# Kernel tuning notes

Measured on AMD Instinct MI355X. Metric: run time of the kernel, lower is better.

## Reference

```python
import jax, jax.numpy as jnp
import numpy as np

B, T, C, H = 2, 2048, 2048, 16
HD = C // H  # 128 head dim
ROPE_BASE = 10000.0


def setup_inputs() -> dict:
    key = jax.random.key(0)
    k0, k1, k2 = jax.random.split(key, 3)
    x = jax.random.normal(k0, (B, T, C), dtype=jnp.float32)
    W_attn = jax.random.normal(k1, (C, 3 * C), dtype=jnp.float32) * 0.02
    b_attn = jnp.zeros((3 * C,), dtype=jnp.float32)
    W_proj = jax.random.normal(k2, (C, C), dtype=jnp.float32) * 0.02
    b_proj = jnp.zeros((C,), dtype=jnp.float32)
    # freqs_cis = exp(i * t * theta_j), represented as (cos, sin), shape [T, HD//2]
    inv_freq = 1.0 / (ROPE_BASE ** (jnp.arange(0, HD, 2, dtype=jnp.float32) / HD))
    freqs = jnp.outer(jnp.arange(T, dtype=jnp.float32), inv_freq)
    return {"x": x, "W_attn": W_attn, "b_attn": b_attn, "W_proj": W_proj,
            "b_proj": b_proj, "cos": jnp.cos(freqs), "sin": jnp.sin(freqs)}


def _apply_rope(v, cos, sin):
    # v: [B, T, H, HD]; pairs (v[..., 2i], v[..., 2i+1]) rotated by angle freqs[t, i]
    vr = v.reshape(v.shape[:-1] + (-1, 2))
    x0, x1 = vr[..., 0], vr[..., 1]
    c = cos[None, :, None, :]  # [1, T, 1, HD//2]
    s = sin[None, :, None, :]
    o0 = x0 * c - x1 * s
    o1 = x0 * s + x1 * c
    return jnp.stack([o0, o1], axis=-1).reshape(v.shape)


def reference(x, W_attn, b_attn, W_proj, b_proj, cos, sin):
    Bv, Tv, Cv = x.shape
    qkv = x @ W_attn + b_attn                      # [B, T, 3C]
    q, k, v = jnp.split(qkv, 3, axis=-1)
    q = q.reshape(Bv, Tv, H, HD)
    k = k.reshape(Bv, Tv, H, HD)
    v = v.reshape(Bv, Tv, H, HD)
    q = _apply_rope(q, cos, sin)
    k = _apply_rope(k, cos, sin)
    scale = 1.0 / jnp.sqrt(jnp.float32(HD))
    att = jnp.einsum('bqhd,bkhd->bhqk', q, k) * scale
    causal = jnp.tril(jnp.ones((Tv, Tv), dtype=bool))
    att = jnp.where(causal[None, None], att, jnp.finfo(att.dtype).min)
    att = jax.nn.softmax(att, axis=-1)
    y = jnp.einsum('bhqk,bkhd->bqhd', att, v).reshape(Bv, Tv, Cv)
    return y @ W_proj + b_proj
```

## Files before the change

kernel.cpp:

```cpp
#include <hip/hip_runtime.h>

typedef unsigned short u16;
typedef __attribute__((ext_vector_type(8))) short short8;
typedef __attribute__((ext_vector_type(4))) float f32x4;

#define TSEQ 2048
#define NHEAD 16
#define HDIM 128

__device__ __forceinline__ u16 f2bf(float x) {
    unsigned u = __float_as_uint(x);
    return (u16)((u + 0x7fffu + ((u >> 16) & 1u)) >> 16);
}
__device__ __forceinline__ float b2f(u16 h) {
    return __uint_as_float(((unsigned)h) << 16);
}
__device__ __forceinline__ void async16(const void* g, void* l) {
    __builtin_amdgcn_global_load_lds((__attribute__((address_space(1))) void*)(void*)g,
                                     (__attribute__((address_space(3))) void*)l, 16, 0, 0);
}
__device__ __forceinline__ f32x4 zero4() {
    f32x4 z = {0.f, 0.f, 0.f, 0.f};
    return z;
}

template <int CTRL>
__device__ __forceinline__ float dppf(float x) {
    return __int_as_float(__builtin_amdgcn_mov_dpp(__float_as_int(x), CTRL, 0xf, 0xf, true));
}
__device__ __forceinline__ float dpp_max16(float x) {
    x = fmaxf(x, dppf<0xB1>(x));
    x = fmaxf(x, dppf<0x4E>(x));
    x = fmaxf(x, dppf<0x141>(x));
    x = fmaxf(x, dppf<0x140>(x));
    return x;
}
__device__ __forceinline__ float dpp_sum16(float x) {
    x += dppf<0xB1>(x);
    x += dppf<0x4E>(x);
    x += dppf<0x141>(x);
    x += dppf<0x140>(x);
    return x;
}

__global__ void cast_bf16(const float4* __restrict__ in, ushort4* __restrict__ out, int n4) {
    int i = blockIdx.x * 256 + threadIdx.x;
    if (i < n4) {
        float4 v = in[i];
        ushort4 o;
        o.x = f2bf(v.x); o.y = f2bf(v.y); o.z = f2bf(v.z); o.w = f2bf(v.w);
        out[i] = o;
    }
}

__global__ void transpose_cast(const float* __restrict__ in, u16* __restrict__ out, int K, int N) {
    __shared__ float tile[64][65];
    int n0 = blockIdx.x * 64, k0 = blockIdx.y * 64;
    int tx = threadIdx.x & 63, ty = threadIdx.x >> 6;
#pragma unroll
    for (int i = 0; i < 16; i++) {
        int r = ty + i * 4;
        tile[r][tx] = in[(size_t)(k0 + r) * N + n0 + tx];
    }
    __syncthreads();
#pragma unroll
    for (int i = 0; i < 16; i++) {
        int r = ty + i * 4;
        out[(size_t)(n0 + r) * K + k0 + tx] = f2bf(tile[tx][r]);
    }
}

template <int MODE>
__global__ __launch_bounds__(256) void gemm_bt(
    const u16* __restrict__ A, const u16* __restrict__ Bt, const float* __restrict__ bias,
    float* __restrict__ outf, u16* __restrict__ qb, u16* __restrict__ kb, u16* __restrict__ vb,
    int M, int N, int K) {
    __shared__ u16 As[128 * 32];
    __shared__ u16 Bs[128 * 32];
    const int tid = threadIdx.x;
    const int wave = tid >> 6, lane = tid & 63;
    const int low = lane & 15, quad = lane >> 4;
    const int m0 = blockIdx.y * 128, n0 = blockIdx.x * 128;
    const int wm = (wave >> 1) * 64, wn = (wave & 1) * 64;
    const int ldr = lane >> 2;
    const int ldc = (lane & 3) * 8;

    f32x4 acc[4][4];
#pragma unroll
    for (int i = 0; i < 4; i++)
#pragma unroll
        for (int j = 0; j < 4; j++) acc[i][j] = zero4();

    for (int k0 = 0; k0 < K; k0 += 32) {
#pragma unroll
        for (int c = 0; c < 2; ++c) {
            const int chunk = wave * 2 + c;
            const int row = chunk * 16 + ldr;
            async16(A + (size_t)(m0 + row) * K + k0 + ldc, As + chunk * 512);
            async16(Bt + (size_t)(n0 + row) * K + k0 + ldc, Bs + chunk * 512);
        }
        __syncthreads();
        short8 af[4], bfv[4];
#pragma unroll
        for (int i = 0; i < 4; i++) af[i] = *(const short8*)(As + (wm + i * 16 + low) * 32 + quad * 8);
#pragma unroll
        for (int j = 0; j < 4; j++) bfv[j] = *(const short8*)(Bs + (wn + j * 16 + low) * 32 + quad * 8);
#pragma unroll
        for (int i = 0; i < 4; i++)
#pragma unroll
            for (int j = 0; j < 4; j++)
                acc[i][j] = __builtin_amdgcn_mfma_f32_16x16x32_bf16(af[i], bfv[j], acc[i][j], 0, 0, 0);
        __syncthreads();
    }

#pragma unroll
    for (int j = 0; j < 4; j++) {
        const int ng = n0 + wn + j * 16 + low;
        const float bv = bias[ng];
#pragma unroll
        for (int i = 0; i < 4; i++) {
            const int rbase = m0 + wm + i * 16 + quad * 4;
#pragma unroll
            for (int r = 0; r < 4; r++) {
                float v = acc[i][j][r] + bv;
                int rowg = rbase + r;
                if (MODE == 1) {
                    outf[(size_t)rowg * N + ng] = v;
                } else {
                    int which = ng >> 11;
                    int hd = ng & 2047;
                    int bq = rowg >> 11, t = rowg & 2047;
                    u16* dst = (which == 0) ? qb : (which == 1) ? kb : vb;
                    dst[(((size_t)(bq * NHEAD + (hd >> 7))) * TSEQ + t) * HDIM + (hd & 127)] = f2bf(v);
                }
            }
        }
    }
}

__global__ void rope_inplace(u16* __restrict__ qb, u16* __restrict__ kb,
                             const float* __restrict__ cosp, const float* __restrict__ sinp) {
    int idx = blockIdx.x * 256 + threadIdx.x;
    int i = idx & 63;
    int bt = idx >> 6;
    int t = bt & (TSEQ - 1);
    size_t o = (size_t)bt * HDIM + 2 * i;
    float c = cosp[t * 64 + i], s = sinp[t * 64 + i];
    float q0 = b2f(qb[o]), q1 = b2f(qb[o + 1]);
    qb[o] = f2bf(q0 * c - q1 * s);
    qb[o + 1] = f2bf(q0 * s + q1 * c);
    float k0 = b2f(kb[o]), k1 = b2f(kb[o + 1]);
    kb[o] = f2bf(k0 * c - k1 * s);
    kb[o + 1] = f2bf(k0 * s + k1 * c);
}

__global__ void vtrans(const u16* __restrict__ vtmp, u16* __restrict__ vT) {
    __shared__ u16 tile[64][66];
    int bid = blockIdx.x;
    int tt = bid & 31;
    int dt = (bid >> 5) & 1;
    int bh = bid >> 6;
    int t0 = tt * 64, d0 = dt * 64;
    int tx = threadIdx.x & 63, ty = threadIdx.x >> 6;
    size_t ibase = ((size_t)bh * TSEQ + t0) * HDIM + d0;
#pragma unroll
    for (int i = 0; i < 16; i++) {
        int r = ty + i * 4;
        tile[r][tx] = vtmp[ibase + (size_t)r * HDIM + tx];
    }
    __syncthreads();
    size_t obase = ((size_t)bh * HDIM + d0) * TSEQ + t0;
#pragma unroll
    for (int i = 0; i < 16; i++) {
        int r = ty + i * 4;
        vT[obase + (size_t)r * TSEQ + tx] = tile[tx][r];
    }
}

__global__ __launch_bounds__(256) void flash_attn(const u16* __restrict__ qb, const u16* __restrict__ kb,
                                                  const u16* __restrict__ vT, u16* __restrict__ y) {
    __shared__ u16 Ks[64 * 128];
    __shared__ u16 Vs[128 * 64];
    __shared__ u16 Ps[4][16 * 72];
    const int tid = threadIdx.x;
    const int wave = tid >> 6, lane = tid & 63;
    const int low = lane & 15, quad = lane >> 4;
    const int bh = blockIdx.x;
    const int qt = 31 - blockIdx.y;
    const int q0 = qt * 64 + wave * 16;
    const float scale2 = 0.08838834764831845f * 1.44269504088896f;

    const u16* Qp = qb + ((size_t)bh * TSEQ + q0) * HDIM;
    short8 qf[4];
#pragma unroll
    for (int c = 0; c < 4; c++) qf[c] = *(const short8*)(Qp + (size_t)low * HDIM + c * 32 + quad * 8);

    f32x4 o[8];
#pragma unroll
    for (int d = 0; d < 8; d++) o[d] = zero4();
    float m_i[4], l_i[4];
#pragma unroll
    for (int r = 0; r < 4; r++) { m_i[r] = -1e30f; l_i[r] = 0.f; }

    const u16* Kb = kb + (size_t)bh * TSEQ * HDIM;
    const u16* Vb = vT + (size_t)bh * HDIM * TSEQ;
    u16* Pw = &Ps[wave][0];
    const int ntiles = qt + 1;

    const int krow = tid >> 4, kchunk = tid & 15;
    const int vrow = tid >> 3, vchunk = tid & 7;

    for (int kt = 0; kt < ntiles; ++kt) {
        const int kv0 = kt * 64;
#pragma unroll
        for (int j = 0; j < 4; j++) {
            const int row = j * 16 + krow;
            const int gc = kchunk ^ (row & 7);
            async16(Kb + (size_t)(kv0 + row) * HDIM + gc * 8, Ks + row * 128 + kchunk * 8);
        }
#pragma unroll
        for (int j = 0; j < 4; j++) {
            const int d = j * 32 + vrow;
            const int gc = vchunk ^ (d & 7);
            async16(Vb + (size_t)d * TSEQ + kv0 + gc * 8, Vs + d * 64 + vchunk * 8);
        }
        __syncthreads();

        f32x4 s[4];
#pragma unroll
        for (int h = 0; h < 4; h++) s[h] = zero4();
#pragma unroll
        for (int h = 0; h < 4; h++) {
            const int row = h * 16 + low;
#pragma unroll
            for (int c = 0; c < 4; c++) {
                const int cc = c * 4 + quad;
                short8 kf = *(const short8*)(Ks + row * 128 + (cc ^ (row & 7)) * 8);
                s[h] = __builtin_amdgcn_mfma_f32_16x16x32_bf16(qf[c], kf, s[h], 0, 0, 0);
            }
        }

        float alpha[4];
#pragma unroll
        for (int r = 0; r < 4; r++) {
            const int qg = q0 + quad * 4 + r;
            float sv[4];
#pragma unroll
            for (int h = 0; h < 4; h++)
                sv[h] = (kv0 + h * 16 + low <= qg) ? s[h][r] * scale2 : -1e30f;
            float mx = fmaxf(fmaxf(sv[0], sv[1]), fmaxf(sv[2], sv[3]));
            mx = dpp_max16(mx);
            float mnew = fmaxf(m_i[r], mx);
            alpha[r] = exp2f(m_i[r] - mnew);
            m_i[r] = mnew;
            float p0 = exp2f(sv[0] - mnew);
            float p1 = exp2f(sv[1] - mnew);
            float p2 = exp2f(sv[2] - mnew);
            float p3 = exp2f(sv[3] - mnew);
            float rs = (p0 + p1) + (p2 + p3);
            rs = dpp_sum16(rs);
            l_i[r] = l_i[r] * alpha[r] + rs;
            const int prow = (quad * 4 + r) * 72;
            Pw[prow + low] = f2bf(p0);
            Pw[prow + 16 + low] = f2bf(p1);
            Pw[prow + 32 + low] = f2bf(p2);
            Pw[prow + 48 + low] = f2bf(p3);
        }
        __threadfence_block();

#pragma unroll
        for (int d = 0; d < 8; ++d)
#pragma unroll
            for (int r = 0; r < 4; r++) o[d][r] *= alpha[r];

#pragma unroll
        for (int kc = 0; kc < 2; kc++) {
            short8 pf = *(const short8*)(Pw + low * 72 + kc * 32 + quad * 8);
#pragma unroll
            for (int dd = 0; dd < 8; ++dd) {
                const int vr = dd * 16 + low;
                const int cc = kc * 4 + quad;
                short8 vf = *(const short8*)(Vs + vr * 64 + (cc ^ (vr & 7)) * 8);
                o[dd] = __builtin_amdgcn_mfma_f32_16x16x32_bf16(pf, vf, o[dd], 0, 0, 0);
            }
        }
        __syncthreads();
    }

    const int b = bh >> 4, h = bh & 15;
#pragma unroll
    for (int r = 0; r < 4; r++) {
        float inv = 1.0f / l_i[r];
        size_t row = (size_t)(b * TSEQ + q0 + quad * 4 + r);
        u16* yp = y + row * 2048 + h * HDIM;
#pragma unroll
        for (int d = 0; d < 8; ++d) yp[d * 16 + low] = f2bf(o[d][r] * inv);
    }
}

extern "C" void kernel_launch(void* const* d_in, const int* in_sizes, int n_in,
                              void* d_out, int out_size, void* d_ws, size_t ws_size,
                              hipStream_t stream) {
    const float* x = (const float*)d_in[0];
    const float* Wa = (const float*)d_in[1];
    const float* ba = (const float*)d_in[2];
    const float* Wp = (const float*)d_in[3];
    const float* bp = (const float*)d_in[4];
    const float* cs = (const float*)d_in[5];
    const float* sn = (const float*)d_in[6];
    float* out = (float*)d_out;

    u16* xb = (u16*)d_ws;
    u16* Wab = xb + 8388608;
    u16* Wpb = Wab + 12582912;
    u16* qb = Wpb + 4194304;
    u16* kb = qb + 8388608;
    u16* vtmp = kb + 8388608;
    u16* vT = vtmp + 8388608;
    u16* y = xb;

    cast_bf16<<<8192, 256, 0, stream>>>((const float4*)x, (ushort4*)xb, 2097152);
    transpose_cast<<<dim3(96, 32), 256, 0, stream>>>(Wa, Wab, 2048, 6144);
    transpose_cast<<<dim3(32, 32), 256, 0, stream>>>(Wp, Wpb, 2048, 2048);
    gemm_bt<0><<<dim3(48, 32), 256, 0, stream>>>(xb, Wab, ba, nullptr, qb, kb, vtmp, 4096, 6144, 2048);
    rope_inplace<<<16384, 256, 0, stream>>>(qb, kb, cs, sn);
    vtrans<<<2048, 256, 0, stream>>>(vtmp, vT);
    flash_attn<<<dim3(32, 32), 256, 0, stream>>>(qb, kb, vT, y);
    gemm_bt<1><<<dim3(16, 32), 256, 0, stream>>>(y, Wpb, bp, out, nullptr, nullptr, nullptr, 4096, 2048, 2048);
}
```

Baseline: 463.7 us.

## Fuse RoPE and V transpose into QKV GEMM epilogue via LDS staging

The QKV GEMM epilogue now stages each 128x128 output tile through shared memory. For Q and K tiles it applies RoPE and writes vectorized 16-byte rows. For V tiles it writes the transposed layout directly. This removes the separate rope_inplace and vtrans kernels, their global round trips, and the vtmp buffer. In exchange the epilogue gains extra barriers, a larger shared-memory footprint, and cos/sin loads inside the GEMM.

```diff
diff --git a/kernel.cpp b/kernel.cpp
--- a/kernel.cpp
+++ b/kernel.cpp
@@ -73,10 +73,12 @@
 template <int MODE>
 __global__ __launch_bounds__(256) void gemm_bt(
     const u16* __restrict__ A, const u16* __restrict__ Bt, const float* __restrict__ bias,
-    float* __restrict__ outf, u16* __restrict__ qb, u16* __restrict__ kb, u16* __restrict__ vb,
+    float* __restrict__ outf, u16* __restrict__ qb, u16* __restrict__ kb, u16* __restrict__ vT,
+    const float* __restrict__ cosp, const float* __restrict__ sinp,
     int M, int N, int K) {
-    __shared__ u16 As[128 * 32];
-    __shared__ u16 Bs[128 * 32];
+    __shared__ __align__(16) u16 smem[8704];
+    u16* As = smem;
+    u16* Bs = smem + 4096;
     const int tid = threadIdx.x;
     const int wave = tid >> 6, lane = tid & 63;
     const int low = lane & 15, quad = lane >> 4;
@@ -113,67 +115,92 @@
         __syncthreads();
     }
 
-#pragma unroll
-    for (int j = 0; j < 4; j++) {
-        const int ng = n0 + wn + j * 16 + low;
-        const float bv = bias[ng];
-#pragma unroll
-        for (int i = 0; i < 4; i++) {
-            const int rbase = m0 + wm + i * 16 + quad * 4;
-#pragma unroll
-            for (int r = 0; r < 4; r++) {
-                float v = acc[i][j][r] + bv;
-                int rowg = rbase + r;
-                if (MODE == 1) {
-                    outf[(size_t)rowg * N + ng] = v;
-                } else {
-                    int which = ng >> 11;
-                    int hd = ng & 2047;
-                    int bq = rowg >> 11, t = rowg & 2047;
-                    u16* dst = (which == 0) ? qb : (which == 1) ? kb : vb;
-                    dst[(((size_t)(bq * NHEAD + (hd >> 7))) * TSEQ + t) * HDIM + (hd & 127)] = f2bf(v);
-                }
-            }
-        }
-    }
-}
-
-__global__ void rope_inplace(u16* __restrict__ qb, u16* __restrict__ kb,
-                             const float* __restrict__ cosp, const float* __restrict__ sinp) {
-    int idx = blockIdx.x * 256 + threadIdx.x;
-    int i = idx & 63;
-    int bt = idx >> 6;
-    int t = bt & (TSEQ - 1);
-    size_t o = (size_t)bt * HDIM + 2 * i;
-    float c = cosp[t * 64 + i], s = sinp[t * 64 + i];
-    float q0 = b2f(qb[o]), q1 = b2f(qb[o + 1]);
-    qb[o] = f2bf(q0 * c - q1 * s);
-    qb[o + 1] = f2bf(q0 * s + q1 * c);
-    float k0 = b2f(kb[o]), k1 = b2f(kb[o + 1]);
-    kb[o] = f2bf(k0 * c - k1 * s);
-    kb[o + 1] = f2bf(k0 * s + k1 * c);
-}
-
-__global__ void vtrans(const u16* __restrict__ vtmp, u16* __restrict__ vT) {
-    __shared__ u16 tile[64][66];
-    int bid = blockIdx.x;
-    int tt = bid & 31;
-    int dt = (bid >> 5) & 1;
-    int bh = bid >> 6;
-    int t0 = tt * 64, d0 = dt * 64;
-    int tx = threadIdx.x & 63, ty = threadIdx.x >> 6;
-    size_t ibase = ((size_t)bh * TSEQ + t0) * HDIM + d0;
-#pragma unroll
-    for (int i = 0; i < 16; i++) {
-        int r = ty + i * 4;
-        tile[r][tx] = vtmp[ibase + (size_t)r * HDIM + tx];
-    }
-    __syncthreads();
-    size_t obase = ((size_t)bh * HDIM + d0) * TSEQ + t0;
-#pragma unroll
-    for (int i = 0; i < 16; i++) {
-        int r = ty + i * 4;
-        vT[obase + (size_t)r * TSEQ + tx] = tile[tx][r];
+    if (MODE == 1) {
+#pragma unroll
+        for (int j = 0; j < 4; j++) {
+            const int ng = n0 + wn + j * 16 + low;
+            const float bv = bias[ng];
+#pragma unroll
+            for (int i = 0; i < 4; i++) {
+                const int rbase = m0 + wm + i * 16 + quad * 4;
+#pragma unroll
+                for (int r = 0; r < 4; r++)
+                    outf[(size_t)(rbase + r) * N + ng] = acc[i][j][r] + bv;
+            }
+        }
+        return;
+    }
+
+    const int which = n0 >> 11;
+    const int h = (n0 & 2047) >> 7;
+    const int b = m0 >> 11, t0 = m0 & 2047;
+    float bv[4];
+#pragma unroll
+    for (int j = 0; j < 4; j++) bv[j] = bias[n0 + wn + j * 16 + low];
+    u16* epi = smem;
+
+    if (which < 2) {
+        u16* dst = (which == 0 ? qb : kb) + (((size_t)(b * NHEAD + h)) * TSEQ + t0) * HDIM;
+#pragma unroll
+        for (int pass = 0; pass < 2; pass++) {
+            if ((wave >> 1) == pass) {
+#pragma unroll
+                for (int i = 0; i < 4; i++)
+#pragma unroll
+                    for (int j = 0; j < 4; j++)
+#pragma unroll
+                        for (int r = 0; r < 4; r++)
+                            epi[(i * 16 + quad * 4 + r) * 136 + wn + j * 16 + low] =
+                                f2bf(acc[i][j][r] + bv[j]);
+            }
+            __syncthreads();
+            const int row = tid >> 2, dp = (tid & 3) * 32;
+            const int t = t0 + pass * 64 + row;
+            u16 vals[32];
+#pragma unroll
+            for (int q = 0; q < 4; q++)
+                *(short8*)(vals + q * 8) = *(const short8*)(epi + row * 136 + dp + q * 8);
+            float cs4[16], sn4[16];
+#pragma unroll
+            for (int q = 0; q < 4; q++) {
+                *(float4*)(cs4 + q * 4) = *(const float4*)(cosp + (size_t)t * 64 + (dp >> 1) + q * 4);
+                *(float4*)(sn4 + q * 4) = *(const float4*)(sinp + (size_t)t * 64 + (dp >> 1) + q * 4);
+            }
+            u16 outv[32];
+#pragma unroll
+            for (int p = 0; p < 16; p++) {
+                float x0 = b2f(vals[2 * p]), x1 = b2f(vals[2 * p + 1]);
+                outv[2 * p] = f2bf(x0 * cs4[p] - x1 * sn4[p]);
+                outv[2 * p + 1] = f2bf(x0 * sn4[p] + x1 * cs4[p]);
+            }
+            u16* dr = dst + (size_t)(pass * 64 + row) * HDIM + dp;
+#pragma unroll
+            for (int q = 0; q < 4; q++)
+                *(short8*)(dr + q * 8) = *(const short8*)(outv + q * 8);
+            __syncthreads();
+        }
+    } else {
+        u16* dst = vT + ((size_t)(b * NHEAD + h)) * HDIM * TSEQ + t0;
+#pragma unroll
+        for (int pass = 0; pass < 2; pass++) {
+            if ((wave & 1) == pass) {
+#pragma unroll
+                for (int i = 0; i < 4; i++)
+#pragma unroll
+                    for (int j = 0; j < 4; j++)
+#pragma unroll
+                        for (int r = 0; r < 4; r++)
+                            epi[(j * 16 + low) * 136 + wm + i * 16 + quad * 4 + r] =
+                                f2bf(acc[i][j][r] + bv[j]);
+            }
+            __syncthreads();
+            const int drow = tid >> 2, tc = (tid & 3) * 32;
+            u16* dr = dst + (size_t)(pass * 64 + drow) * TSEQ + tc;
+#pragma unroll
+            for (int q = 0; q < 4; q++)
+                *(short8*)(dr + q * 8) = *(const short8*)(epi + drow * 136 + tc + q * 8);
+            __syncthreads();
+        }
     }
 }
 
@@ -315,16 +342,13 @@
     u16* Wpb = Wab + 12582912;
     u16* qb = Wpb + 4194304;
     u16* kb = qb + 8388608;
-    u16* vtmp = kb + 8388608;
-    u16* vT = vtmp + 8388608;
+    u16* vT = kb + 8388608;
     u16* y = xb;
 
     cast_bf16<<<8192, 256, 0, stream>>>((const float4*)x, (ushort4*)xb, 2097152);
     transpose_cast<<<dim3(96, 32), 256, 0, stream>>>(Wa, Wab, 2048, 6144);
     transpose_cast<<<dim3(32, 32), 256, 0, stream>>>(Wp, Wpb, 2048, 2048);
-    gemm_bt<0><<<dim3(48, 32), 256, 0, stream>>>(xb, Wab, ba, nullptr, qb, kb, vtmp, 4096, 6144, 2048);
-    rope_inplace<<<16384, 256, 0, stream>>>(qb, kb, cs, sn);
-    vtrans<<<2048, 256, 0, stream>>>(vtmp, vT);
+    gemm_bt<0><<<dim3(48, 32), 256, 0, stream>>>(xb, Wab, ba, nullptr, qb, kb, vT, cs, sn, 4096, 6144, 2048);
     flash_attn<<<dim3(32, 32), 256, 0, stream>>>(qb, kb, vT, y);
-    gemm_bt<1><<<dim3(16, 32), 256, 0, stream>>>(y, Wpb, bp, out, nullptr, nullptr, nullptr, 4096, 2048, 2048);
-}
+    gemm_bt<1><<<dim3(16, 32), 256, 0, stream>>>(y, Wpb, bp, out, nullptr, nullptr, nullptr, nullptr, nullptr, 4096, 2048, 2048);
+}
```

Result: no change. 455.6 us (-1.8%).
